# Kernel tuning notes

Hardware: AMD Instinct MI355X
Metric: run time of the kernel (lower is better)

Reference implementation:

```python
import jax, jax.numpy as jnp
import numpy as np

B, T, D = 2, 1024, 2048
HK, HV, DK, DV = 16, 32, 128, 128
KCONV = 4
INTER = 8192
EPS = 1e-6
KEY_DIM = HK * DK          # 2048
VAL_DIM = HV * DV          # 4096
CONV_DIM = 2 * KEY_DIM + VAL_DIM  # 8192


def setup_inputs() -> dict:
    key = jax.random.key(0)
    ks = jax.random.split(key, 16)
    s = 0.02
    return {
        "positions": jnp.broadcast_to(jnp.arange(T, dtype=jnp.int32), (B, T)),
        "hidden_states": jax.random.normal(ks[0], (B, T, D), jnp.float32),
        "residual": jax.random.normal(ks[1], (B, T, D), jnp.float32),
        "ln_in_w": jnp.zeros((D,), jnp.float32),
        "ln_post_w": jnp.zeros((D,), jnp.float32),
        "Wqkvz": jax.random.normal(ks[2], (D, 2 * KEY_DIM + 2 * VAL_DIM), jnp.float32) * s,
        "Wba": jax.random.normal(ks[3], (D, 2 * HV), jnp.float32) * s,
        "conv_w": jax.random.normal(ks[4], (CONV_DIM, KCONV), jnp.float32) * 0.1,
        "A_log": jnp.log(jax.random.uniform(ks[5], (HV,), jnp.float32, 1.0, 16.0)),
        "dt_bias": jax.random.normal(ks[6], (HV,), jnp.float32) * 0.1,
        "norm_w": jnp.ones((DV,), jnp.float32),
        "Wout": jax.random.normal(ks[7], (VAL_DIM, D), jnp.float32) * s,
        "Wgate": jax.random.normal(ks[8], (D, INTER), jnp.float32) * s,
        "Wup": jax.random.normal(ks[9], (D, INTER), jnp.float32) * s,
        "Wdown": jax.random.normal(ks[10], (INTER, D), jnp.float32) * s,
    }


def _gemma_rmsnorm(x, w):
    xf = x.astype(jnp.float32)
    v = jnp.mean(xf * xf, axis=-1, keepdims=True)
    return (xf * jax.lax.rsqrt(v + EPS) * (1.0 + w)).astype(x.dtype)


def _causal_depthwise_conv(x, w):
    # x: [B,T,C], w: [C,K]; causal depthwise conv1d
    Kw = w.shape[1]
    Tlen = x.shape[1]
    xp = jnp.pad(x, ((0, 0), (Kw - 1, 0), (0, 0)))
    return sum(xp[:, i:i + Tlen, :] * w[:, i] for i in range(Kw))


def _l2norm(x):
    return x * jax.lax.rsqrt(jnp.sum(x * x, axis=-1, keepdims=True) + 1e-6)


def reference(positions, hidden_states, residual, ln_in_w, ln_post_w, Wqkvz, Wba,
              conv_w, A_log, dt_bias, norm_w, Wout, Wgate, Wup, Wdown):
    b, t, d = hidden_states.shape
    # fused input RMSNorm + residual add
    res1 = hidden_states + residual
    h = _gemma_rmsnorm(res1, ln_in_w)

    # ---- GatedDeltaNet linear attention ----
    qkvz = h @ Wqkvz
    q, k, v, z = jnp.split(qkvz, [KEY_DIM, 2 * KEY_DIM, 2 * KEY_DIM + VAL_DIM], axis=-1)
    ba = h @ Wba
    bb, aa = jnp.split(ba, [HV], axis=-1)  # [b,t,HV] each

    qkv = jax.nn.silu(_causal_depthwise_conv(jnp.concatenate([q, k, v], axis=-1), conv_w))
    q, k, v = jnp.split(qkv, [KEY_DIM, 2 * KEY_DIM], axis=-1)

    q = _l2norm(q.reshape(b, t, HK, DK))
    k = _l2norm(k.reshape(b, t, HK, DK))
    v = v.reshape(b, t, HV, DV)
    z = z.reshape(b, t, HV, DV)
    rep = HV // HK
    q = jnp.repeat(q, rep, axis=2) * (DK ** -0.5)  # [b,t,HV,DK]
    k = jnp.repeat(k, rep, axis=2)

    beta = jax.nn.sigmoid(bb)                              # [b,t,HV]
    decay = jnp.exp(-jnp.exp(A_log) * jax.nn.softplus(aa + dt_bias))  # [b,t,HV]

    def step(S, xs):
        q_t, k_t, v_t, b_t, d_t = xs  # [b,HV,DK],[b,HV,DK],[b,HV,DV],[b,HV],[b,HV]
        S = S * d_t[..., None, None]
        v_pred = jnp.einsum('bhk,bhkv->bhv', k_t, S)
        delta = (v_t - v_pred) * b_t[..., None]
        S = S + jnp.einsum('bhk,bhv->bhkv', k_t, delta)
        o = jnp.einsum('bhk,bhkv->bhv', q_t, S)
        return S, o

    xs = (q.transpose(1, 0, 2, 3), k.transpose(1, 0, 2, 3), v.transpose(1, 0, 2, 3),
          beta.transpose(1, 0, 2), decay.transpose(1, 0, 2))
    S0 = jnp.zeros((b, HV, DK, DV), dtype=q.dtype)
    _, o = jax.lax.scan(step, S0, xs)
    o = o.transpose(1, 0, 2, 3)  # [b,t,HV,DV]

    # gated per-head RMSNorm: gate first (Qwen3-Next style), then normalize
    og = (o * jax.nn.silu(z)).astype(jnp.float32)
    var = jnp.mean(og * og, axis=-1, keepdims=True)
    og = (og * jax.lax.rsqrt(var + EPS)) * norm_w
    attn = og.reshape(b, t, VAL_DIM).astype(h.dtype) @ Wout

    # fused post-attention RMSNorm + residual
    res2 = attn + res1
    h2 = _gemma_rmsnorm(res2, ln_post_w)

    # gated SiLU MLP
    out = (jax.nn.silu(h2 @ Wgate) * (h2 @ Wup)) @ Wdown
    return (out, res2)
```

## Files before the change

kernel.cpp:

```cpp
#include <hip/hip_runtime.h>
#include <hip/hip_bf16.h>

typedef unsigned short u16;
typedef unsigned int u32;
typedef float f32x4 __attribute__((ext_vector_type(4)));
typedef short bf16x8 __attribute__((ext_vector_type(8)));
typedef unsigned short u16x4 __attribute__((ext_vector_type(4)));
typedef unsigned int u32x2 __attribute__((ext_vector_type(2)));
typedef unsigned int u32x4 __attribute__((ext_vector_type(4)));

#define BT 2048
#define DMODEL 2048
#define HV 32
#define DK 128
#define KEYDIM 2048
#define VALDIM 4096
#define QKVZ_N 12288
#define CONVC 8192
#define INTER 8192

__device__ __forceinline__ float bf2f(u16 v) {
  u32 u = ((u32)v) << 16;
  return __builtin_bit_cast(float, u);
}
__device__ __forceinline__ u16 f2bf(float f) {
  u32 u = __builtin_bit_cast(u32, f);
  u32 r = (u + 0x7fffu + ((u >> 16) & 1u)) >> 16;
  return (u16)r;
}
__device__ __forceinline__ u32 pack2(float a, float b) {
  return (u32)f2bf(a) | ((u32)f2bf(b) << 16);
}
__device__ __forceinline__ float siluf(float x) {
  return x / (1.f + expf(-x));
}

__global__ __launch_bounds__(256) void convert_transpose(
    const float* __restrict__ W, int ldw, u16* __restrict__ Wt, int K, int N) {
  __shared__ float tileT[64][68];
  int n0 = blockIdx.x * 64, k0 = blockIdx.y * 64;
  int tx = threadIdx.x & 15, ty = threadIdx.x >> 4;
#pragma unroll
  for (int i = 0; i < 4; ++i) {
    int kk = ty + i * 16;
    f32x4 v = *(const f32x4*)(W + (size_t)(k0 + kk) * ldw + n0 + tx * 4);
#pragma unroll
    for (int j = 0; j < 4; ++j) tileT[tx * 4 + j][kk] = v[j];
  }
  __syncthreads();
#pragma unroll
  for (int i = 0; i < 4; ++i) {
    int nn = ty + i * 16;
    f32x4 v = *(const f32x4*)(&tileT[nn][tx * 4]);
    u16x4 st;
#pragma unroll
    for (int j = 0; j < 4; ++j) st[j] = f2bf(v[j]);
    *(u16x4*)(Wt + (size_t)(n0 + nn) * K + k0 + tx * 4) = st;
  }
}

__global__ __launch_bounds__(256) void resnorm_kernel(
    const float* __restrict__ a, const float* __restrict__ b,
    const float* __restrict__ w, float* __restrict__ resout,
    u16* __restrict__ hb) {
  int tok = blockIdx.x, t = threadIdx.x;
  const float* ap = a + (size_t)tok * DMODEL + t * 8;
  const float* bp = b + (size_t)tok * DMODEL + t * 8;
  f32x4 x0 = *(const f32x4*)ap + *(const f32x4*)bp;
  f32x4 x1 = *(const f32x4*)(ap + 4) + *(const f32x4*)(bp + 4);
  *(f32x4*)(resout + (size_t)tok * DMODEL + t * 8) = x0;
  *(f32x4*)(resout + (size_t)tok * DMODEL + t * 8 + 4) = x1;
  float ss = 0.f;
#pragma unroll
  for (int j = 0; j < 4; ++j) ss += x0[j] * x0[j] + x1[j] * x1[j];
#pragma unroll
  for (int m = 1; m < 64; m <<= 1) ss += __shfl_xor(ss, m, 64);
  __shared__ float red[4];
  if ((t & 63) == 0) red[t >> 6] = ss;
  __syncthreads();
  ss = red[0] + red[1] + red[2] + red[3];
  float sc = rsqrtf(ss * (1.f / (float)DMODEL) + 1e-6f);
  const float* wp = w + t * 8;
  float y[8];
#pragma unroll
  for (int j = 0; j < 4; ++j) {
    y[j] = x0[j] * sc * (1.f + wp[j]);
    y[4 + j] = x1[j] * sc * (1.f + wp[4 + j]);
  }
  u32x4 st;
  st[0] = pack2(y[0], y[1]);
  st[1] = pack2(y[2], y[3]);
  st[2] = pack2(y[4], y[5]);
  st[3] = pack2(y[6], y[7]);
  *(u32x4*)(hb + (size_t)tok * DMODEL + t * 8) = st;
}

__global__ __launch_bounds__(256) void resnorm2_kernel(
    const float* __restrict__ p, const float* __restrict__ b,
    const float* __restrict__ w, float* __restrict__ resout,
    u16* __restrict__ hb) {
  int tok = blockIdx.x, t = threadIdx.x;
  size_t base = (size_t)tok * DMODEL + t * 8;
  const float* p0 = p + base;
  const float* p1 = p + (size_t)BT * DMODEL + base;
  const float* bp = b + base;
  f32x4 x0 = *(const f32x4*)p0 + *(const f32x4*)p1 + *(const f32x4*)bp;
  f32x4 x1 = *(const f32x4*)(p0 + 4) + *(const f32x4*)(p1 + 4) +
             *(const f32x4*)(bp + 4);
  *(f32x4*)(resout + base) = x0;
  *(f32x4*)(resout + base + 4) = x1;
  float ss = 0.f;
#pragma unroll
  for (int j = 0; j < 4; ++j) ss += x0[j] * x0[j] + x1[j] * x1[j];
#pragma unroll
  for (int m = 1; m < 64; m <<= 1) ss += __shfl_xor(ss, m, 64);
  __shared__ float red[4];
  if ((t & 63) == 0) red[t >> 6] = ss;
  __syncthreads();
  ss = red[0] + red[1] + red[2] + red[3];
  float sc = rsqrtf(ss * (1.f / (float)DMODEL) + 1e-6f);
  const float* wp = w + t * 8;
  float y[8];
#pragma unroll
  for (int j = 0; j < 4; ++j) {
    y[j] = x0[j] * sc * (1.f + wp[j]);
    y[4 + j] = x1[j] * sc * (1.f + wp[4 + j]);
  }
  u32x4 st;
  st[0] = pack2(y[0], y[1]);
  st[1] = pack2(y[2], y[3]);
  st[2] = pack2(y[4], y[5]);
  st[3] = pack2(y[6], y[7]);
  *(u32x4*)(hb + base) = st;
}

__device__ __forceinline__ void async16(const void* g, void* l) {
  __builtin_amdgcn_global_load_lds(
      (const __attribute__((address_space(1))) u32*)g,
      (__attribute__((address_space(3))) u32*)l, 16, 0, 0);
}

template <int OUT>
__global__ __launch_bounds__(256) void gemm_kernel(
    const u16* __restrict__ A, const u16* __restrict__ Bt,
    void* __restrict__ Cv, const u16* __restrict__ Aux, int M, int N,
    int Kfull, int Ks) {
  __shared__ __align__(16) u16 Al[4][128 * 32];
  __shared__ __align__(16) u16 Bl[4][128 * 32];
  int tid = threadIdx.x;
  int w = tid >> 6, l = tid & 63;
  int wr = w >> 1, wc = w & 1;
  int r15 = l & 15, kb = l >> 4;

  int nbx = gridDim.x, nby = gridDim.y;
  int bid = blockIdx.y * nbx + blockIdx.x;
  int nwg = nbx * nby;
  int cpx = nwg >> 3;
  int wg = (bid & 7) * cpx + (bid >> 3);
  const int GRP = 4;
  int span = GRP * nby;
  int grpId = wg / span;
  int rem = wg - grpId * span;
  int n0 = (grpId * GRP + (rem % GRP)) * 128;
  int m0 = (rem / GRP) * 128;
  int kbase = blockIdx.z * Ks;

  f32x4 acc[4][4] = {};

  const u16* baseA[2];
  const u16* baseB[2];
#pragma unroll
  for (int c = 0; c < 2; ++c) {
    int gid = w * 128 + c * 64 + l;
    int row = gid >> 2;
    int g = (gid & 3) ^ ((row >> 1) & 3);
    baseA[c] = A + (size_t)(m0 + row) * Kfull + kbase + g * 8;
    baseB[c] = Bt + (size_t)(n0 + row) * Kfull + kbase + g * 8;
  }
  auto stage = [&](int buf, int koff) {
#pragma unroll
    for (int c = 0; c < 2; ++c) {
      int gid = w * 128 + c * 64 + l;
      async16(baseA[c] + koff, Al[buf] + gid * 8);
      async16(baseB[c] + koff, Bl[buf] + gid * 8);
    }
  };

  int nst = Ks >> 5;
#pragma unroll
  for (int p = 0; p < 3; ++p)
    if (p < nst) stage(p & 3, p * 32);

  for (int i = 0; i < nst; ++i) {
    int issued = (i + 3 < nst) ? (i + 3) : nst;
    int infl = issued - i - 1;
    if (infl >= 2)
      asm volatile("s_waitcnt vmcnt(8)" ::: "memory");
    else if (infl == 1)
      asm volatile("s_waitcnt vmcnt(4)" ::: "memory");
    else
      asm volatile("s_waitcnt vmcnt(0)" ::: "memory");
    __builtin_amdgcn_s_barrier();
    __builtin_amdgcn_sched_barrier(0);
    if (i + 3 < nst) stage((i + 3) & 3, (i + 3) * 32);
    const u16* Ac = Al[i & 3];
    const u16* Bc = Bl[i & 3];
    bf16x8 aF[4], bF[4];
#pragma unroll
    for (int m = 0; m < 4; ++m) {
      int row = wr * 64 + m * 16 + r15;
      aF[m] = *(const bf16x8*)(Ac + row * 32 + (kb ^ ((row >> 1) & 3)) * 8);
    }
#pragma unroll
    for (int n = 0; n < 4; ++n) {
      int row = wc * 64 + n * 16 + r15;
      bF[n] = *(const bf16x8*)(Bc + row * 32 + (kb ^ ((row >> 1) & 3)) * 8);
    }
#pragma unroll
    for (int m = 0; m < 4; ++m)
#pragma unroll
      for (int n = 0; n < 4; ++n)
        acc[m][n] = __builtin_amdgcn_mfma_f32_16x16x32_bf16(aF[m], bF[n],
                                                            acc[m][n], 0, 0, 0);
  }

  float* Cf = (float*)Cv + (size_t)blockIdx.z * M * N;
#pragma unroll
  for (int m = 0; m < 4; ++m)
#pragma unroll
    for (int n = 0; n < 4; ++n) {
      size_t base = (size_t)(m0 + wr * 64 + m * 16 + kb * 4) * N +
                    (n0 + wc * 64 + n * 16 + r15);
#pragma unroll
      for (int r = 0; r < 4; ++r) {
        size_t idx = base + (size_t)r * N;
        if (OUT == 0)
          Cf[idx] = acc[m][n][r];
        else if (OUT == 1)
          ((u16*)Cv)[idx] = f2bf(acc[m][n][r]);
        else
          ((u16*)Cv)[idx] = f2bf(siluf(bf2f(Aux[idx])) * acc[m][n][r]);
      }
    }
}

template <int OUT>
__global__ __launch_bounds__(1024, 1) void gemm1024_kernel(
    const u16* __restrict__ A, const u16* __restrict__ Bt,
    void* __restrict__ Cv, const u16* __restrict__ Aux, int M, int N,
    int Kfull, int Ks) {
  __shared__ __align__(16) u16 S[65536];
  int tid = threadIdx.x;
  int l = tid & 63, w = tid >> 6;
  int wm = w >> 2, wn = w & 3;
  int r15 = l & 15, kb = l >> 4;

  int nbx = gridDim.x, nby = gridDim.y;
  int bid = blockIdx.y * nbx + blockIdx.x;
  int nwg = nbx * nby;
  int cpx = nwg >> 3;
  int wg = (bid & 7) * cpx + (bid >> 3);
  const int GRP = 4;
  int span = GRP * nby;
  int grpId = wg / span;
  int rem = wg - grpId * span;
  int n0 = (grpId * GRP + (rem % GRP)) * 256;
  int m0 = (rem / GRP) * 256;
  int kbase = blockIdx.z * Ks;

  f32x4 acc[4][4] = {};

  int srow = tid >> 2, sgg = tid & 3;
  int sgl = sgg ^ ((srow >> 1) & 3);
  const u16* baseA = A + (size_t)(m0 + srow) * Kfull + kbase + sgl * 8;
  const u16* baseB = Bt + (size_t)(n0 + srow) * Kfull + kbase + sgl * 8;

  int nt = Ks >> 6;
#pragma unroll
  for (int kh = 0; kh < 2; ++kh) {
    async16(baseA + kh * 32, S + ((0 * 2 + 0) * 2 + kh) * 8192 + tid * 8);
    async16(baseB + kh * 32, S + ((0 * 2 + 1) * 2 + kh) * 8192 + tid * 8);
  }
  asm volatile("s_waitcnt vmcnt(2)" ::: "memory");
  __builtin_amdgcn_s_barrier();

  for (int t = 0; t < nt; ++t) {
    int buf = t & 1;
    bool hn = t + 1 < nt;
    int koff = (t + 1) * 64;
#pragma unroll
    for (int kh = 0; kh < 2; ++kh) {
      const u16* Ac = S + ((buf * 2 + 0) * 2 + kh) * 8192;
      const u16* Bc = S + ((buf * 2 + 1) * 2 + kh) * 8192;
      bf16x8 aF[4], bF[4];
#pragma unroll
      for (int m = 0; m < 4; ++m) {
        int row = wm * 64 + m * 16 + r15;
        aF[m] = *(const bf16x8*)(Ac + row * 32 + (kb ^ ((row >> 1) & 3)) * 8);
      }
#pragma unroll
      for (int n = 0; n < 4; ++n) {
        int row = wn * 64 + n * 16 + r15;
        bF[n] = *(const bf16x8*)(Bc + row * 32 + (kb ^ ((row >> 1) & 3)) * 8);
      }
      if (hn) {
        async16(baseA + koff + kh * 32,
                S + (((buf ^ 1) * 2 + 0) * 2 + kh) * 8192 + tid * 8);
        async16(baseB + koff + kh * 32,
                S + (((buf ^ 1) * 2 + 1) * 2 + kh) * 8192 + tid * 8);
      }
      asm volatile("s_waitcnt lgkmcnt(0)" ::: "memory");
      __builtin_amdgcn_sched_barrier(0);
      __builtin_amdgcn_s_setprio(1);
#pragma unroll
      for (int m = 0; m < 4; ++m)
#pragma unroll
        for (int n = 0; n < 4; ++n)
          acc[m][n] = __builtin_amdgcn_mfma_f32_16x16x32_bf16(
              aF[m], bF[n], acc[m][n], 0, 0, 0);
      __builtin_amdgcn_s_setprio(0);
      if (hn)
        asm volatile("s_waitcnt vmcnt(2)" ::: "memory");
      else if (kh == 0)
        asm volatile("s_waitcnt vmcnt(0)" ::: "memory");
      __builtin_amdgcn_s_barrier();
    }
  }

  float* Cf = (float*)Cv + (size_t)blockIdx.z * M * N;
#pragma unroll
  for (int m = 0; m < 4; ++m)
#pragma unroll
    for (int n = 0; n < 4; ++n) {
      size_t base = (size_t)(m0 + wm * 64 + m * 16 + kb * 4) * N +
                    (n0 + wn * 64 + n * 16 + r15);
#pragma unroll
      for (int r = 0; r < 4; ++r) {
        size_t idx = base + (size_t)r * N;
        if (OUT == 0)
          Cf[idx] = acc[m][n][r];
        else if (OUT == 1)
          ((u16*)Cv)[idx] = f2bf(acc[m][n][r]);
        else
          ((u16*)Cv)[idx] = f2bf(siluf(bf2f(Aux[idx])) * acc[m][n][r]);
      }
    }
}

__global__ __launch_bounds__(256) void reduce_kernel(
    const float* __restrict__ p, float* __restrict__ o, int n, int S) {
  int i = (blockIdx.x * 256 + threadIdx.x) * 4;
  f32x4 s = *(const f32x4*)(p + i);
  for (int j = 1; j < S; ++j) s += *(const f32x4*)(p + (size_t)j * n + i);
  *(f32x4*)(o + i) = s;
}

__global__ __launch_bounds__(256) void ba_bd_kernel(
    const u16* __restrict__ hb, const float* __restrict__ Wba,
    const float* __restrict__ A_log, const float* __restrict__ dt_bias,
    float* __restrict__ bd) {
  int m = blockIdx.x;
  int t = threadIdx.x;
  int n = t & 63, kq = t >> 6;
  const u16* a = hb + (size_t)m * DMODEL + kq * 512;
  const float* wp = Wba + (size_t)kq * 512 * 64 + n;
  float sum = 0.f;
  for (int i = 0; i < 512; ++i)
    sum += bf2f(a[i]) * wp[(size_t)i * 64];
  __shared__ float red[256];
  red[t] = sum;
  __syncthreads();
  if (t < 32) {
    float bb = red[t] + red[t + 64] + red[t + 128] + red[t + 192];
    float aa = red[t + 32] + red[t + 96] + red[t + 160] + red[t + 224];
    float bet = 1.f / (1.f + expf(-bb));
    float x = aa + dt_bias[t];
    float sp = (x > 20.f) ? x : log1pf(expf(x));
    float dec = expf(-expf(A_log[t]) * sp);
    int b = m >> 10, tt = m & 1023;
    size_t o = (((size_t)(b * 32 + t)) * 1024 + tt) * 2;
    bd[o] = bet;
    bd[o + 1] = dec;
  }
}

__global__ __launch_bounds__(256) void conv_l2_kernel(
    const u16* __restrict__ qkvb, const float* __restrict__ conv_w,
    u16* __restrict__ qkv) {
  int tok = blockIdx.x;
  int b = tok >> 10, tt = tok & 1023;
  int t = threadIdx.x;
  int c0 = t * 32;
  float acc[32];
  {
    bf16x8 x[4][4];
    bool valid[4];
#pragma unroll
    for (int i = 0; i < 4; ++i) {
      int ts = tt - 3 + i;
      valid[i] = ts >= 0;
      const u16* rp = qkvb + (size_t)(b * 1024 + (valid[i] ? ts : 0)) * CONVC + c0;
#pragma unroll
      for (int gq = 0; gq < 4; ++gq) x[i][gq] = *(const bf16x8*)(rp + gq * 8);
    }
#pragma unroll
    for (int gq = 0; gq < 4; ++gq)
#pragma unroll
      for (int j = 0; j < 8; ++j) {
        f32x4 wv = *(const f32x4*)(conv_w + (c0 + gq * 8 + j) * 4);
        float s = 0.f;
#pragma unroll
        for (int i = 0; i < 4; ++i)
          if (valid[i]) s = fmaf(bf2f((u16)x[i][gq][j]), wv[i], s);
        acc[gq * 8 + j] = siluf(s);
      }
  }
  if (t < 128) {
    float ss = 1e-6f;
#pragma unroll
    for (int j = 0; j < 32; ++j) ss += acc[j] * acc[j];
    ss += __shfl_xor(ss, 1, 64);
    ss += __shfl_xor(ss, 2, 64);
    ss -= 3e-6f;
    float sc = rsqrtf(ss);
    if (t < 64) sc *= 0.08838834764831845f;
#pragma unroll
    for (int j = 0; j < 32; ++j) acc[j] *= sc;
  }
  u16* op = qkv + (size_t)tok * CONVC + c0;
#pragma unroll
  for (int gq = 0; gq < 4; ++gq) {
    u32x4 st;
#pragma unroll
    for (int p2 = 0; p2 < 4; ++p2)
      st[p2] = pack2(acc[gq * 8 + p2 * 2], acc[gq * 8 + p2 * 2 + 1]);
    *(u32x4*)(op + gq * 8) = st;
  }
}

__global__ __launch_bounds__(256) void prep_kernel(
    const u16* __restrict__ qkvc, const float* __restrict__ bdpack,
    u16* __restrict__ Tg, u16* __restrict__ Pg, u16* __restrict__ KtTg,
    float* __restrict__ Bvec) {
  __shared__ __align__(16) u16 Kl[64 * 128];
  __shared__ __align__(16) u16 Ql[64 * 128];
  __shared__ __align__(16) float Af[64 * 65];
  __shared__ float bl[64], betal[64], sc63[64];
  int tid = threadIdx.x;
  int w = tid >> 6, l = tid & 63;
  int r15 = l & 15, kb = l >> 4;
  int c = blockIdx.x, bh = blockIdx.y;
  int b = bh >> 5, h = bh & 31, hk = h >> 1;
  size_t tok0 = (size_t)b * 1024 + c * 64;
  int ch = bh * 16 + c;

#pragma unroll
  for (int rep = 0; rep < 4; ++rep) {
    int gid = w * 256 + rep * 64 + l;
    int row = gid >> 4, seg = gid & 15;
    const u16* srcq = qkvc + (tok0 + row) * CONVC + hk * 128 + seg * 8;
    async16(srcq, Ql + gid * 8);
    async16(srcq + KEYDIM, Kl + gid * 8);
  }
  if (tid < 64) {
    size_t o = ((size_t)bh * 1024 + c * 64 + tid) * 2;
    betal[tid] = bdpack[o];
    float s = logf(fmaxf(bdpack[o + 1], 1e-30f));
#pragma unroll
    for (int d = 1; d < 64; d <<= 1) {
      float t = __shfl_up(s, d, 64);
      if (tid >= d) s += t;
    }
    bl[tid] = s;
    float tot = __shfl(s, 63, 64);
    sc63[tid] = expf(tot - s);
    Bvec[(size_t)ch * 64 + tid] = expf(s);
  }
  __syncthreads();

  {
    f32x4 akk[4] = {}, aqk[4] = {};
#pragma unroll
    for (int ks = 0; ks < 4; ++ks) {
      bf16x8 kaF = *(const bf16x8*)(Kl + (w * 16 + r15) * 128 + ks * 32 + kb * 8);
      bf16x8 qaF = *(const bf16x8*)(Ql + (w * 16 + r15) * 128 + ks * 32 + kb * 8);
#pragma unroll
      for (int n = 0; n < 4; ++n) {
        bf16x8 bF = *(const bf16x8*)(Kl + (n * 16 + r15) * 128 + ks * 32 + kb * 8);
        akk[n] = __builtin_amdgcn_mfma_f32_16x16x32_bf16(kaF, bF, akk[n], 0, 0, 0);
        aqk[n] = __builtin_amdgcn_mfma_f32_16x16x32_bf16(qaF, bF, aqk[n], 0, 0, 0);
      }
    }
#pragma unroll
    for (int n = 0; n < 4; ++n)
#pragma unroll
      for (int r = 0; r < 4; ++r) {
        int i = w * 16 + kb * 4 + r;
        int j = n * 16 + r15;
        float e = expf(bl[i] - bl[j]);
        Af[i * 65 + j] = (j < i) ? betal[i] * e * akk[n][r] : 0.f;
        u16 pv = (j <= i) ? f2bf(e * aqk[n][r]) : (u16)0;
        Pg[(size_t)ch * 4096 + i * 64 + j] = pv;
      }
  }
  for (int m = 0; m < 32; ++m) {
    int idx = tid * 32 + m;
    int d = idx >> 6, j = idx & 63;
    KtTg[(size_t)ch * 8192 + idx] = f2bf(bf2f(Kl[j * 128 + d]) * sc63[j]);
  }
  __syncthreads();

  {
    int ccol = w * 16 + r15;
    float tj[16];
#pragma unroll
    for (int m = 0; m < 16; ++m) tj[m] = (4 * m + kb == ccol) ? 1.f : 0.f;
#pragma unroll
    for (int i = 1; i < 64; ++i) {
      float part = 0.f;
      const int mb = (i + 3) >> 2;
#pragma unroll
      for (int m = 0; m < 16; ++m)
        if (m < mb) part = fmaf(Af[i * 65 + 4 * m + kb], tj[m], part);
      part += __shfl_xor(part, 16, 64);
      part += __shfl_xor(part, 32, 64);
      float nv = ((ccol == i) ? 1.f : 0.f) - part;
      if (kb == (i & 3)) tj[i >> 2] = nv;
    }
#pragma unroll
    for (int m = 0; m < 16; ++m)
      Tg[(size_t)ch * 4096 + (4 * m + kb) * 64 + ccol] = f2bf(tj[m]);
  }
}

__global__ __launch_bounds__(512) void chunk_scan_kernel(
    const u16* __restrict__ qkvc, const float* __restrict__ bdpack,
    const u16* __restrict__ Tg, const u16* __restrict__ Pg,
    const u16* __restrict__ KtTg, const float* __restrict__ Bvec,
    u16* __restrict__ obf) {
  __shared__ __align__(16) u16 Kl[64 * 128];
  __shared__ __align__(16) u16 Ql[64 * 128];
  __shared__ __align__(16) u16 KtTl[128 * 64];
  __shared__ __align__(16) u16 Tl[64 * 64];
  __shared__ __align__(16) u16 Pl[64 * 64];
  __shared__ __align__(16) u16 Vl[64 * 32];
  __shared__ __align__(16) u16 St[32 * 128];
  __shared__ __align__(16) u16 rhsT[32 * 64];
  __shared__ __align__(16) u16 dT[32 * 64];
  __shared__ float betal[64], Gl[64];

  int tid = threadIdx.x;
  int w = tid >> 6, l = tid & 63;
  int r15 = l & 15, kb = l >> 4;
  int dvc = blockIdx.x, bh = blockIdx.y;
  int b = bh >> 5, h = bh & 31, hk = h >> 1;
  int a = w >> 1, bcol = w & 1;

  for (int m = tid; m < 32 * 128; m += 512) St[m] = 0;
  f32x4 sAcc0 = {}, sAcc1 = {};
  __syncthreads();

  for (int c = 0; c < 16; ++c) {
    size_t tok0 = (size_t)b * 1024 + c * 64;
    int ch = bh * 16 + c;
#pragma unroll
    for (int rep = 0; rep < 2; ++rep) {
      int gid = w * 128 + rep * 64 + l;
      int row = gid >> 4, seg = gid & 15;
      const u16* srcq = qkvc + (tok0 + row) * CONVC + hk * 128 + seg * 8;
      async16(srcq, Ql + gid * 8);
      async16(srcq + KEYDIM, Kl + gid * 8);
      async16(KtTg + (size_t)ch * 8192 + gid * 8, KtTl + gid * 8);
    }
    {
      int gid = w * 64 + l;
      async16(Tg + (size_t)ch * 4096 + gid * 8, Tl + gid * 8);
      async16(Pg + (size_t)ch * 4096 + gid * 8, Pl + gid * 8);
    }
    if (w < 4) {
      int gid = w * 64 + l;
      int row = gid >> 2, seg = gid & 3;
      async16(qkvc + (tok0 + row) * CONVC + 2 * KEYDIM + h * 128 + dvc * 32 + seg * 8,
              Vl + gid * 8);
    }
    if (tid < 64) {
      betal[tid] = bdpack[((size_t)bh * 1024 + c * 64 + tid) * 2];
      Gl[tid] = Bvec[(size_t)ch * 64 + tid];
    }
    __syncthreads();

    f32x4 aKS = {}, aQS = {};
#pragma unroll
    for (int ks = 0; ks < 4; ++ks) {
      bf16x8 bF = *(const bf16x8*)(St + (bcol * 16 + r15) * 128 + ks * 32 + kb * 8);
      bf16x8 kF = *(const bf16x8*)(Kl + (a * 16 + r15) * 128 + ks * 32 + kb * 8);
      bf16x8 qF = *(const bf16x8*)(Ql + (a * 16 + r15) * 128 + ks * 32 + kb * 8);
      aKS = __builtin_amdgcn_mfma_f32_16x16x32_bf16(kF, bF, aKS, 0, 0, 0);
      aQS = __builtin_amdgcn_mfma_f32_16x16x32_bf16(qF, bF, aQS, 0, 0, 0);
    }
    {
      int i0 = a * 16 + kb * 4;
      int dv = bcol * 16 + r15;
      u16x4 st;
#pragma unroll
      for (int r = 0; r < 4; ++r) {
        int i = i0 + r;
        float v = bf2f(Vl[i * 32 + dv]);
        st[r] = f2bf(betal[i] * (v - Gl[i] * aKS[r]));
      }
      *(u16x4*)(rhsT + dv * 64 + i0) = st;
    }
    __syncthreads();
    f32x4 aD = {};
#pragma unroll
    for (int ks = 0; ks < 2; ++ks) {
      bf16x8 aF = *(const bf16x8*)(Tl + (a * 16 + r15) * 64 + ks * 32 + kb * 8);
      bf16x8 bF = *(const bf16x8*)(rhsT + (bcol * 16 + r15) * 64 + ks * 32 + kb * 8);
      aD = __builtin_amdgcn_mfma_f32_16x16x32_bf16(aF, bF, aD, 0, 0, 0);
    }
    {
      int i0 = a * 16 + kb * 4;
      int dv = bcol * 16 + r15;
      u16x4 st;
#pragma unroll
      for (int r = 0; r < 4; ++r) st[r] = f2bf(aD[r]);
      *(u16x4*)(dT + dv * 64 + i0) = st;
    }
    __syncthreads();
    f32x4 aO = {};
#pragma unroll
    for (int ks = 0; ks < 2; ++ks) {
      bf16x8 aF = *(const bf16x8*)(Pl + (a * 16 + r15) * 64 + ks * 32 + kb * 8);
      bf16x8 bF = *(const bf16x8*)(dT + (bcol * 16 + r15) * 64 + ks * 32 + kb * 8);
      aO = __builtin_amdgcn_mfma_f32_16x16x32_bf16(aF, bF, aO, 0, 0, 0);
    }
    {
      int i0 = a * 16 + kb * 4;
      int dv = bcol * 16 + r15;
#pragma unroll
      for (int r = 0; r < 4; ++r) {
        int i = i0 + r;
        float o = aO[r] + Gl[i] * aQS[r];
        obf[(tok0 + i) * VALDIM + h * 128 + dvc * 32 + dv] = f2bf(o);
      }
    }
    float gL = Gl[63];
#pragma unroll
    for (int r = 0; r < 4; ++r) { sAcc0[r] *= gL; sAcc1[r] *= gL; }
#pragma unroll
    for (int ks = 0; ks < 2; ++ks) {
      bf16x8 aF = *(const bf16x8*)(KtTl + (w * 16 + r15) * 64 + ks * 32 + kb * 8);
      bf16x8 b0 = *(const bf16x8*)(dT + r15 * 64 + ks * 32 + kb * 8);
      bf16x8 b1 = *(const bf16x8*)(dT + (16 + r15) * 64 + ks * 32 + kb * 8);
      sAcc0 = __builtin_amdgcn_mfma_f32_16x16x32_bf16(aF, b0, sAcc0, 0, 0, 0);
      sAcc1 = __builtin_amdgcn_mfma_f32_16x16x32_bf16(aF, b1, sAcc1, 0, 0, 0);
    }
#pragma unroll
    for (int r = 0; r < 4; ++r) {
      int dk = w * 16 + kb * 4 + r;
      St[r15 * 128 + dk] = f2bf(sAcc0[r]);
      St[(16 + r15) * 128 + dk] = f2bf(sAcc1[r]);
    }
    __syncthreads();
  }
}

__global__ __launch_bounds__(256) void gatenorm_kernel(
    const u16* __restrict__ obf, u16* __restrict__ zb,
    const float* __restrict__ norm_w) {
  int wid = blockIdx.x * 4 + (threadIdx.x >> 6);
  int l = threadIdx.x & 63;
  int tok = wid >> 5, h = wid & 31;
  const u16* op = obf + (size_t)tok * VALDIM + h * 128 + l * 2;
  u16* zp = zb + (size_t)tok * VALDIM + h * 128 + l * 2;
  float o0 = bf2f(op[0]), o1 = bf2f(op[1]);
  float z0 = bf2f(zp[0]), z1 = bf2f(zp[1]);
  float g0 = o0 * siluf(z0);
  float g1 = o1 * siluf(z1);
  float ss = g0 * g0 + g1 * g1;
#pragma unroll
  for (int m = 1; m < 64; m <<= 1) ss += __shfl_xor(ss, m, 64);
  float sc = rsqrtf(ss * (1.f / 128.f) + 1e-6f);
  int e = l * 2;
  *(u32*)zp = pack2(g0 * sc * norm_w[e], g1 * sc * norm_w[e + 1]);
}

__global__ void diag_kernel(float* out, float val) { out[0] = val; }

extern "C" void kernel_launch(void* const* d_in, const int* in_sizes, int n_in,
                              void* d_out, int out_size, void* d_ws,
                              size_t ws_size, hipStream_t stream) {
  const float* hidden = (const float*)d_in[1];
  const float* residual = (const float*)d_in[2];
  const float* ln_in_w = (const float*)d_in[3];
  const float* ln_post_w = (const float*)d_in[4];
  const float* Wqkvz = (const float*)d_in[5];
  const float* Wba = (const float*)d_in[6];
  const float* conv_w = (const float*)d_in[7];
  const float* A_log = (const float*)d_in[8];
  const float* dt_bias = (const float*)d_in[9];
  const float* norm_w = (const float*)d_in[10];
  const float* Wout = (const float*)d_in[11];
  const float* Wgate = (const float*)d_in[12];
  const float* Wup = (const float*)d_in[13];
  const float* Wdown = (const float*)d_in[14];

  char* ws = (char*)d_ws;
  size_t off = 0;
  auto alloc = [&](size_t n) {
    char* p = ws + off;
    off = (off + n + 255) & ~(size_t)255;
    return p;
  };
  u16* wslot = (u16*)alloc((size_t)INTER * DMODEL * 2);
  u16* hb = (u16*)alloc((size_t)BT * DMODEL * 2);
  u16* qkvb = (u16*)alloc((size_t)BT * CONVC * 2);
  u16* zb = (u16*)alloc((size_t)BT * VALDIM * 2);
  u16* qkvc = (u16*)alloc((size_t)BT * CONVC * 2);
  float* Bvec = (float*)alloc((size_t)1024 * 64 * 4);
  float* bdpack = (float*)alloc((size_t)64 * 1024 * 2 * 4);
  u16* obf = (u16*)alloc((size_t)BT * VALDIM * 2);
  if (off > ws_size) {
    diag_kernel<<<1, 1, 0, stream>>>((float*)d_out, (float)(ws_size >> 20));
    return;
  }

  float* res1 = (float*)d_out;
  float* res2 = (float*)d_out + (size_t)BT * DMODEL;
  u16* h2b = hb;
  u16* gbuf = qkvc;
  u16* mbuf = qkvb;
  float* outp = (float*)d_out;

  u16* Tg = qkvb;
  u16* Pg = qkvb + (size_t)1024 * 4096;
  u16* KtTg = qkvb + (size_t)2 * 1024 * 4096;

  float* pWout = (float*)qkvb;
  float* pDown = (float*)zb;

  dim3 blk(256);
  dim3 blk1024(1024);

  resnorm_kernel<<<BT, blk, 0, stream>>>(hidden, residual, ln_in_w, res1, hb);

  convert_transpose<<<dim3(CONVC / 64, DMODEL / 64), blk, 0, stream>>>(
      Wqkvz, QKVZ_N, wslot, DMODEL, CONVC);
  gemm1024_kernel<1><<<dim3(CONVC / 256, BT / 256), blk1024, 0, stream>>>(
      hb, wslot, qkvb, nullptr, BT, CONVC, DMODEL, DMODEL);

  convert_transpose<<<dim3(VALDIM / 64, DMODEL / 64), blk, 0, stream>>>(
      Wqkvz + CONVC, QKVZ_N, wslot, DMODEL, VALDIM);
  gemm_kernel<1><<<dim3(VALDIM / 128, BT / 128), blk, 0, stream>>>(
      hb, wslot, zb, nullptr, BT, VALDIM, DMODEL, DMODEL);

  ba_bd_kernel<<<BT, blk, 0, stream>>>(hb, Wba, A_log, dt_bias, bdpack);

  conv_l2_kernel<<<BT, blk, 0, stream>>>(qkvb, conv_w, qkvc);

  prep_kernel<<<dim3(16, 64), blk, 0, stream>>>(qkvc, bdpack, Tg, Pg, KtTg,
                                                Bvec);
  chunk_scan_kernel<<<dim3(4, 64), dim3(512), 0, stream>>>(
      qkvc, bdpack, Tg, Pg, KtTg, Bvec, obf);

  gatenorm_kernel<<<BT * HV / 4, blk, 0, stream>>>(obf, zb, norm_w);

  convert_transpose<<<dim3(DMODEL / 64, VALDIM / 64), blk, 0, stream>>>(
      Wout, DMODEL, wslot, VALDIM, DMODEL);
  gemm_kernel<0><<<dim3(DMODEL / 128, BT / 128, 2), blk, 0, stream>>>(
      zb, wslot, pWout, nullptr, BT, DMODEL, VALDIM, VALDIM / 2);

  resnorm2_kernel<<<BT, blk, 0, stream>>>(pWout, res1, ln_post_w, res2, h2b);

  convert_transpose<<<dim3(INTER / 64, DMODEL / 64), blk, 0, stream>>>(
      Wgate, INTER, wslot, DMODEL, INTER);
  gemm1024_kernel<1><<<dim3(INTER / 256, BT / 256), blk1024, 0, stream>>>(
      h2b, wslot, gbuf, nullptr, BT, INTER, DMODEL, DMODEL);

  convert_transpose<<<dim3(INTER / 64, DMODEL / 64), blk, 0, stream>>>(
      Wup, INTER, wslot, DMODEL, INTER);
  gemm1024_kernel<2><<<dim3(INTER / 256, BT / 256), blk1024, 0, stream>>>(
      h2b, wslot, mbuf, gbuf, BT, INTER, DMODEL, DMODEL);

  convert_transpose<<<dim3(DMODEL / 64, INTER / 64), blk, 0, stream>>>(
      Wdown, DMODEL, wslot, INTER, DMODEL);
  gemm1024_kernel<0><<<dim3(DMODEL / 256, BT / 256, 4), blk1024, 0, stream>>>(
      mbuf, wslot, pDown, nullptr, BT, DMODEL, INTER, INTER / 4);
  reduce_kernel<<<BT * DMODEL / 1024, blk, 0, stream>>>(pDown, outp,
                                                        BT * DMODEL, 4);
}
```

Before: 787.6 us.

## XOR-swizzle LDS tiles in chunk scan and split conv/l2norm kernel

Applies an XOR swizzle (segment ^ row&7) to the Q, K, KtT, T, P, St, rhsT and dT shared-memory tiles in prep and chunk_scan kernels, so MFMA fragment reads hit different LDS banks instead of conflicting. The global-to-LDS copies and the stores are permuted to match. It also splits the fused conv+SiLU+L2 kernel into a finer-grained conv_silu kernel plus a separate per-head l2norm kernel. The split adds an extra launch and another read/write pass over the q/k region.

```diff
diff --git a/kernel.cpp b/kernel.cpp
--- a/kernel.cpp
+++ b/kernel.cpp
@@ -384,58 +384,44 @@
   }
 }
 
-__global__ __launch_bounds__(256) void conv_l2_kernel(
+__global__ __launch_bounds__(256) void conv_silu_kernel(
     const u16* __restrict__ qkvb, const float* __restrict__ conv_w,
     u16* __restrict__ qkv) {
-  int tok = blockIdx.x;
-  int b = tok >> 10, tt = tok & 1023;
-  int t = threadIdx.x;
-  int c0 = t * 32;
-  float acc[32];
-  {
-    bf16x8 x[4][4];
-    bool valid[4];
-#pragma unroll
-    for (int i = 0; i < 4; ++i) {
-      int ts = tt - 3 + i;
-      valid[i] = ts >= 0;
-      const u16* rp = qkvb + (size_t)(b * 1024 + (valid[i] ? ts : 0)) * CONVC + c0;
-#pragma unroll
-      for (int gq = 0; gq < 4; ++gq) x[i][gq] = *(const bf16x8*)(rp + gq * 8);
-    }
-#pragma unroll
-    for (int gq = 0; gq < 4; ++gq)
-#pragma unroll
-      for (int j = 0; j < 8; ++j) {
-        f32x4 wv = *(const f32x4*)(conv_w + (c0 + gq * 8 + j) * 4);
-        float s = 0.f;
-#pragma unroll
-        for (int i = 0; i < 4; ++i)
-          if (valid[i]) s = fmaf(bf2f((u16)x[i][gq][j]), wv[i], s);
-        acc[gq * 8 + j] = siluf(s);
-      }
-  }
-  if (t < 128) {
-    float ss = 1e-6f;
-#pragma unroll
-    for (int j = 0; j < 32; ++j) ss += acc[j] * acc[j];
-    ss += __shfl_xor(ss, 1, 64);
-    ss += __shfl_xor(ss, 2, 64);
-    ss -= 3e-6f;
-    float sc = rsqrtf(ss);
-    if (t < 64) sc *= 0.08838834764831845f;
-#pragma unroll
-    for (int j = 0; j < 32; ++j) acc[j] *= sc;
-  }
-  u16* op = qkv + (size_t)tok * CONVC + c0;
-#pragma unroll
-  for (int gq = 0; gq < 4; ++gq) {
-    u32x4 st;
-#pragma unroll
-    for (int p2 = 0; p2 < 4; ++p2)
-      st[p2] = pack2(acc[gq * 8 + p2 * 2], acc[gq * 8 + p2 * 2 + 1]);
-    *(u32x4*)(op + gq * 8) = st;
-  }
+  int gid = blockIdx.x * 256 + threadIdx.x;
+  int c4 = (gid & 2047) * 4;
+  int bt = gid >> 11;
+  int b = bt >> 10, tt = bt & 1023;
+  f32x4 wv[4];
+#pragma unroll
+  for (int j = 0; j < 4; ++j) wv[j] = *(const f32x4*)(conv_w + (c4 + j) * 4);
+  float acc[4] = {0.f, 0.f, 0.f, 0.f};
+#pragma unroll
+  for (int i = 0; i < 4; ++i) {
+    int ts = tt - 3 + i;
+    if (ts >= 0) {
+      u16x4 x = *(const u16x4*)(qkvb + (size_t)(b * 1024 + ts) * CONVC + c4);
+#pragma unroll
+      for (int j = 0; j < 4; ++j) acc[j] += bf2f(x[j]) * wv[j][i];
+    }
+  }
+  u32x2 st;
+  st[0] = pack2(siluf(acc[0]), siluf(acc[1]));
+  st[1] = pack2(siluf(acc[2]), siluf(acc[3]));
+  *(u32x2*)(qkv + (size_t)bt * CONVC + c4) = st;
+}
+
+__global__ __launch_bounds__(256) void l2norm_kernel(u16* __restrict__ qkv) {
+  int wid = blockIdx.x * 4 + (threadIdx.x >> 6);
+  int l = threadIdx.x & 63;
+  int tok = wid >> 5, slot = wid & 31;
+  u16* p = qkv + (size_t)tok * CONVC + slot * 128 + l * 2;
+  float x0 = bf2f(p[0]), x1 = bf2f(p[1]);
+  float ss = x0 * x0 + x1 * x1;
+#pragma unroll
+  for (int m = 1; m < 64; m <<= 1) ss += __shfl_xor(ss, m, 64);
+  float sc = rsqrtf(ss + 1e-6f);
+  if (slot < 16) sc *= 0.08838834764831845f;
+  *(u32*)p = pack2(x0 * sc, x1 * sc);
 }
 
 __global__ __launch_bounds__(256) void prep_kernel(
@@ -458,7 +444,8 @@
   for (int rep = 0; rep < 4; ++rep) {
     int gid = w * 256 + rep * 64 + l;
     int row = gid >> 4, seg = gid & 15;
-    const u16* srcq = qkvc + (tok0 + row) * CONVC + hk * 128 + seg * 8;
+    int sseg = seg ^ (row & 7);
+    const u16* srcq = qkvc + (tok0 + row) * CONVC + hk * 128 + sseg * 8;
     async16(srcq, Ql + gid * 8);
     async16(srcq + KEYDIM, Kl + gid * 8);
   }
@@ -482,11 +469,15 @@
     f32x4 akk[4] = {}, aqk[4] = {};
 #pragma unroll
     for (int ks = 0; ks < 4; ++ks) {
-      bf16x8 kaF = *(const bf16x8*)(Kl + (w * 16 + r15) * 128 + ks * 32 + kb * 8);
-      bf16x8 qaF = *(const bf16x8*)(Ql + (w * 16 + r15) * 128 + ks * 32 + kb * 8);
+      int rowa = w * 16 + r15;
+      int ga = ((ks * 4 + kb) ^ (rowa & 7)) * 8;
+      bf16x8 kaF = *(const bf16x8*)(Kl + rowa * 128 + ga);
+      bf16x8 qaF = *(const bf16x8*)(Ql + rowa * 128 + ga);
 #pragma unroll
       for (int n = 0; n < 4; ++n) {
-        bf16x8 bF = *(const bf16x8*)(Kl + (n * 16 + r15) * 128 + ks * 32 + kb * 8);
+        int rowb = n * 16 + r15;
+        int gb = ((ks * 4 + kb) ^ (rowb & 7)) * 8;
+        bf16x8 bF = *(const bf16x8*)(Kl + rowb * 128 + gb);
         akk[n] = __builtin_amdgcn_mfma_f32_16x16x32_bf16(kaF, bF, akk[n], 0, 0, 0);
         aqk[n] = __builtin_amdgcn_mfma_f32_16x16x32_bf16(qaF, bF, aqk[n], 0, 0, 0);
       }
@@ -506,7 +497,8 @@
   for (int m = 0; m < 32; ++m) {
     int idx = tid * 32 + m;
     int d = idx >> 6, j = idx & 63;
-    KtTg[(size_t)ch * 8192 + idx] = f2bf(bf2f(Kl[j * 128 + d]) * sc63[j]);
+    int sidx = j * 128 + (((d >> 3) ^ (j & 7)) * 8) + (d & 7);
+    KtTg[(size_t)ch * 8192 + idx] = f2bf(bf2f(Kl[sidx]) * sc63[j]);
   }
   __syncthreads();
 
@@ -566,16 +558,26 @@
 #pragma unroll
     for (int rep = 0; rep < 2; ++rep) {
       int gid = w * 128 + rep * 64 + l;
-      int row = gid >> 4, seg = gid & 15;
-      const u16* srcq = qkvc + (tok0 + row) * CONVC + hk * 128 + seg * 8;
-      async16(srcq, Ql + gid * 8);
-      async16(srcq + KEYDIM, Kl + gid * 8);
-      async16(KtTg + (size_t)ch * 8192 + gid * 8, KtTl + gid * 8);
+      {
+        int row = gid >> 4, seg = gid & 15;
+        int sseg = seg ^ (row & 7);
+        const u16* srcq = qkvc + (tok0 + row) * CONVC + hk * 128 + sseg * 8;
+        async16(srcq, Ql + gid * 8);
+        async16(srcq + KEYDIM, Kl + gid * 8);
+      }
+      {
+        int row = gid >> 3, seg = gid & 7;
+        int sseg = seg ^ (row & 7);
+        async16(KtTg + (size_t)ch * 8192 + (row * 8 + sseg) * 8,
+                KtTl + gid * 8);
+      }
     }
     {
       int gid = w * 64 + l;
-      async16(Tg + (size_t)ch * 4096 + gid * 8, Tl + gid * 8);
-      async16(Pg + (size_t)ch * 4096 + gid * 8, Pl + gid * 8);
+      int row = gid >> 3, seg = gid & 7;
+      int sseg = seg ^ (row & 7);
+      async16(Tg + (size_t)ch * 4096 + (row * 8 + sseg) * 8, Tl + gid * 8);
+      async16(Pg + (size_t)ch * 4096 + (row * 8 + sseg) * 8, Pl + gid * 8);
     }
     if (w < 4) {
       int gid = w * 64 + l;
@@ -592,9 +594,13 @@
     f32x4 aKS = {}, aQS = {};
 #pragma unroll
     for (int ks = 0; ks < 4; ++ks) {
-      bf16x8 bF = *(const bf16x8*)(St + (bcol * 16 + r15) * 128 + ks * 32 + kb * 8);
-      bf16x8 kF = *(const bf16x8*)(Kl + (a * 16 + r15) * 128 + ks * 32 + kb * 8);
-      bf16x8 qF = *(const bf16x8*)(Ql + (a * 16 + r15) * 128 + ks * 32 + kb * 8);
+      int rowS = bcol * 16 + r15;
+      int gS = ((ks * 4 + kb) ^ (rowS & 7)) * 8;
+      bf16x8 bF = *(const bf16x8*)(St + rowS * 128 + gS);
+      int rowK = a * 16 + r15;
+      int gK = ((ks * 4 + kb) ^ (rowK & 7)) * 8;
+      bf16x8 kF = *(const bf16x8*)(Kl + rowK * 128 + gK);
+      bf16x8 qF = *(const bf16x8*)(Ql + rowK * 128 + gK);
       aKS = __builtin_amdgcn_mfma_f32_16x16x32_bf16(kF, bF, aKS, 0, 0, 0);
       aQS = __builtin_amdgcn_mfma_f32_16x16x32_bf16(qF, bF, aQS, 0, 0, 0);
     }
@@ -608,14 +614,19 @@
         float v = bf2f(Vl[i * 32 + dv]);
         st[r] = f2bf(betal[i] * (v - Gl[i] * aKS[r]));
       }
-      *(u16x4*)(rhsT + dv * 64 + i0) = st;
+      int g = (i0 >> 3) ^ (dv & 7);
+      *(u16x4*)(rhsT + dv * 64 + g * 8 + (i0 & 7)) = st;
     }
     __syncthreads();
     f32x4 aD = {};
 #pragma unroll
     for (int ks = 0; ks < 2; ++ks) {
-      bf16x8 aF = *(const bf16x8*)(Tl + (a * 16 + r15) * 64 + ks * 32 + kb * 8);
-      bf16x8 bF = *(const bf16x8*)(rhsT + (bcol * 16 + r15) * 64 + ks * 32 + kb * 8);
+      int rowT = a * 16 + r15;
+      int gT = ((ks * 4 + kb) ^ (rowT & 7)) * 8;
+      bf16x8 aF = *(const bf16x8*)(Tl + rowT * 64 + gT);
+      int rowR = bcol * 16 + r15;
+      int gR = ((ks * 4 + kb) ^ (rowR & 7)) * 8;
+      bf16x8 bF = *(const bf16x8*)(rhsT + rowR * 64 + gR);
       aD = __builtin_amdgcn_mfma_f32_16x16x32_bf16(aF, bF, aD, 0, 0, 0);
     }
     {
@@ -624,14 +635,19 @@
       u16x4 st;
 #pragma unroll
       for (int r = 0; r < 4; ++r) st[r] = f2bf(aD[r]);
-      *(u16x4*)(dT + dv * 64 + i0) = st;
+      int g = (i0 >> 3) ^ (dv & 7);
+      *(u16x4*)(dT + dv * 64 + g * 8 + (i0 & 7)) = st;
     }
     __syncthreads();
     f32x4 aO = {};
 #pragma unroll
     for (int ks = 0; ks < 2; ++ks) {
-      bf16x8 aF = *(const bf16x8*)(Pl + (a * 16 + r15) * 64 + ks * 32 + kb * 8);
-      bf16x8 bF = *(const bf16x8*)(dT + (bcol * 16 + r15) * 64 + ks * 32 + kb * 8);
+      int rowP = a * 16 + r15;
+      int gP = ((ks * 4 + kb) ^ (rowP & 7)) * 8;
+      bf16x8 aF = *(const bf16x8*)(Pl + rowP * 64 + gP);
+      int rowD = bcol * 16 + r15;
+      int gD = ((ks * 4 + kb) ^ (rowD & 7)) * 8;
+      bf16x8 bF = *(const bf16x8*)(dT + rowD * 64 + gD);
       aO = __builtin_amdgcn_mfma_f32_16x16x32_bf16(aF, bF, aO, 0, 0, 0);
     }
     {
@@ -649,17 +665,24 @@
     for (int r = 0; r < 4; ++r) { sAcc0[r] *= gL; sAcc1[r] *= gL; }
 #pragma unroll
     for (int ks = 0; ks < 2; ++ks) {
-      bf16x8 aF = *(const bf16x8*)(KtTl + (w * 16 + r15) * 64 + ks * 32 + kb * 8);
-      bf16x8 b0 = *(const bf16x8*)(dT + r15 * 64 + ks * 32 + kb * 8);
-      bf16x8 b1 = *(const bf16x8*)(dT + (16 + r15) * 64 + ks * 32 + kb * 8);
+      int rowKt = w * 16 + r15;
+      int gKt = ((ks * 4 + kb) ^ (rowKt & 7)) * 8;
+      bf16x8 aF = *(const bf16x8*)(KtTl + rowKt * 64 + gKt);
+      int row0 = r15, row1 = 16 + r15;
+      int g0 = ((ks * 4 + kb) ^ (row0 & 7)) * 8;
+      int g1 = ((ks * 4 + kb) ^ (row1 & 7)) * 8;
+      bf16x8 b0 = *(const bf16x8*)(dT + row0 * 64 + g0);
+      bf16x8 b1 = *(const bf16x8*)(dT + row1 * 64 + g1);
       sAcc0 = __builtin_amdgcn_mfma_f32_16x16x32_bf16(aF, b0, sAcc0, 0, 0, 0);
       sAcc1 = __builtin_amdgcn_mfma_f32_16x16x32_bf16(aF, b1, sAcc1, 0, 0, 0);
     }
 #pragma unroll
     for (int r = 0; r < 4; ++r) {
       int dk = w * 16 + kb * 4 + r;
-      St[r15 * 128 + dk] = f2bf(sAcc0[r]);
-      St[(16 + r15) * 128 + dk] = f2bf(sAcc1[r]);
+      int g0 = (dk >> 3) ^ (r15 & 7);
+      int g1 = (dk >> 3) ^ ((16 + r15) & 7);
+      St[r15 * 128 + g0 * 8 + (dk & 7)] = f2bf(sAcc0[r]);
+      St[(16 + r15) * 128 + g1 * 8 + (dk & 7)] = f2bf(sAcc1[r]);
     }
     __syncthreads();
   }
@@ -756,7 +779,8 @@
 
   ba_bd_kernel<<<BT, blk, 0, stream>>>(hb, Wba, A_log, dt_bias, bdpack);
 
-  conv_l2_kernel<<<BT, blk, 0, stream>>>(qkvb, conv_w, qkvc);
+  conv_silu_kernel<<<BT * 2048 / 256, blk, 0, stream>>>(qkvb, conv_w, qkvc);
+  l2norm_kernel<<<BT * 32 / 4, blk, 0, stream>>>(qkvc);
 
   prep_kernel<<<dim3(16, 64), blk, 0, stream>>>(qkvc, bdpack, Tg, Pg, KtTg,
                                                 Bvec);
```

Result: faster. 724.9 us, median of 2 (-8.0%).
